# Optimization experiments

Hardware: AMD Instinct MI355X
Metric: run time of the kernel (lower is better)

## Reference

```python
import jax, jax.numpy as jnp
import numpy as np

N, DIM = 8192, 128

def setup_inputs() -> dict:
    key = jax.random.key(0)
    ks = jax.random.split(key, 9)
    s = 1.0 / np.sqrt(DIM)
    return {
        "x": jax.random.normal(ks[0], (N, DIM), dtype=jnp.float32),
        "Wq": jax.random.uniform(ks[1], (DIM, DIM), jnp.float32, -s, s),
        "bq": jax.random.uniform(ks[2], (DIM,), jnp.float32, -s, s),
        "Wk": jax.random.uniform(ks[3], (DIM, DIM), jnp.float32, -s, s),
        "bk": jax.random.uniform(ks[4], (DIM,), jnp.float32, -s, s),
        "Wv": jax.random.uniform(ks[5], (DIM, DIM), jnp.float32, -s, s),
        "bv": jax.random.uniform(ks[6], (DIM,), jnp.float32, -s, s),
        "Wo": jax.random.uniform(ks[7], (DIM, DIM), jnp.float32, -s, s),
        "bo": jax.random.uniform(ks[8], (DIM,), jnp.float32, -s, s),
    }

def reference(x, Wq, bq, Wk, bk, Wv, bv, Wo, bo):
    # nn.Linear: y = x @ W.T + b
    Q = x @ Wq.T + bq                      # [N, d]
    K = x @ Wk.T + bk                      # [N, d]
    V = x @ Wv.T + bv                      # [N, d]
    scale = 1.0 / jnp.sqrt(jnp.asarray(x.shape[-1], x.dtype))
    scores = (Q @ K.T) * scale             # [N, N] — matches original O(n^2) math
    attn = jax.nn.softmax(scores, axis=-1)
    out = attn @ V                         # [N, d]
    return out @ Wo.T + bo
```

## Files before the change

### kernel.cpp

```cpp
#include <hip/hip_runtime.h>
#include <math.h>


typedef __bf16 bf16x8 __attribute__((ext_vector_type(8)));
typedef float f32x4 __attribute__((ext_vector_type(4)));
typedef float f32x16 __attribute__((ext_vector_type(16)));
typedef unsigned int u32x4 __attribute__((ext_vector_type(4)));
typedef unsigned int u32x2 __attribute__((ext_vector_type(2)));
typedef unsigned short us16;

#define NTOK 8192
#define CHUNKS 8

static constexpr float SCALE_L2E = 0.08838834764831845f * 1.4426950408889634f;

__device__ __forceinline__ unsigned f2bf_u(float x) {
    unsigned u = __builtin_bit_cast(unsigned, x);
    return (u + 0x7FFFu + ((u >> 16) & 1u)) >> 16;
}

__device__ __forceinline__ unsigned pk_bf16(float x, float y) {
    unsigned a = __builtin_bit_cast(unsigned, x) + 0x8000u;
    unsigned b = __builtin_bit_cast(unsigned, y) + 0x8000u;
#if __has_builtin(__builtin_amdgcn_perm)
    return __builtin_amdgcn_perm(b, a, 0x07060302u);
#else
    return (a >> 16) | (b & 0xFFFF0000u);
#endif
}

__device__ __forceinline__ unsigned cvtpk_bf16(float x, float y) {
    unsigned r;
    asm("v_cvt_pk_bf16_f32 %0, %1, %2" : "=v"(r) : "v"(x), "v"(y));
    return r;
}

__device__ __forceinline__ void plswap(unsigned& a, unsigned& b) {
    asm("v_permlane32_swap_b32 %0, %1" : "+v"(a), "+v"(b));
}

__device__ __forceinline__ void pl16swap(unsigned& a, unsigned& b) {
    asm("v_permlane16_swap_b32 %0, %1" : "+v"(a), "+v"(b));
}

__device__ __forceinline__ float fexp2(float x) {
#if __has_builtin(__builtin_amdgcn_exp2f)
    return __builtin_amdgcn_exp2f(x);
#else
    return exp2f(x);
#endif
}

__device__ __forceinline__ bf16x8 ld_frag(const us16* p) {
    u32x4 u = *reinterpret_cast<const u32x4*>(p);
    return __builtin_bit_cast(bf16x8, u);
}

__device__ __forceinline__ bf16x8 cvt_frag(const float* p) {
    f32x4 a = *reinterpret_cast<const f32x4*>(p);
    f32x4 b = *reinterpret_cast<const f32x4*>(p + 4);
    u32x4 o;
    o[0] = f2bf_u(a[0]) | (f2bf_u(a[1]) << 16);
    o[1] = f2bf_u(a[2]) | (f2bf_u(a[3]) << 16);
    o[2] = f2bf_u(b[0]) | (f2bf_u(b[1]) << 16);
    o[3] = f2bf_u(b[2]) | (f2bf_u(b[3]) << 16);
    return __builtin_bit_cast(bf16x8, o);
}

__global__ __launch_bounds__(256) void proj_qkv(
    const float* __restrict__ x,
    const float* __restrict__ wq, const float* __restrict__ bq,
    const float* __restrict__ wk, const float* __restrict__ bk,
    const float* __restrict__ wv, const float* __restrict__ bv,
    us16* __restrict__ Qb, us16* __restrict__ Kb, us16* __restrict__ Vt)
{
    __shared__ us16 ldsT[4][16 * 136];

    int z = blockIdx.x >> 7;
    int tile = blockIdx.x & 127;
    const float* W = z == 0 ? wq : z == 1 ? wk : wv;
    const float* bias = z == 0 ? bq : z == 1 ? bk : bv;
    float osc = z == 0 ? SCALE_L2E : 1.0f;

    int w = threadIdx.x >> 6, lane = threadIdx.x & 63;
    int quad = lane >> 4, l15 = lane & 15;
    int rbase = tile * 64 + w * 16;

    bf16x8 af[4];
#pragma unroll
    for (int ks = 0; ks < 4; ++ks)
        af[ks] = cvt_frag(x + (rbase + l15) * 128 + ks * 32 + quad * 8);

    f32x4 acc[8];
#pragma unroll
    for (int nt = 0; nt < 8; ++nt) acc[nt] = f32x4{0.f, 0.f, 0.f, 0.f};

#pragma unroll
    for (int nt = 0; nt < 8; ++nt) {
#pragma unroll
        for (int ks = 0; ks < 4; ++ks) {
            bf16x8 bf = cvt_frag(W + (nt * 16 + l15) * 128 + ks * 32 + quad * 8);
            acc[nt] = __builtin_amdgcn_mfma_f32_16x16x32_bf16(af[ks], bf, acc[nt], 0, 0, 0);
        }
    }

    if (z < 2) {
        us16* T = &ldsT[w][0];
        us16* Out = z == 0 ? Qb : Kb;
#pragma unroll
        for (int nt = 0; nt < 8; ++nt) {
            float bb = bias[nt * 16 + l15];
#pragma unroll
            for (int r = 0; r < 4; ++r)
                T[(quad * 4 + r) * 136 + nt * 16 + l15] =
                    (us16)f2bf_u((acc[nt][r] + bb) * osc);
        }
        asm volatile("s_waitcnt lgkmcnt(0)" ::: "memory");
        __builtin_amdgcn_sched_barrier(0);
        int row = lane >> 2, seg = lane & 3;
        const us16* src = T + row * 136 + seg * 32;
        us16* dst = Out + (rbase + row) * 128 + seg * 32;
#pragma unroll
        for (int c = 0; c < 4; ++c)
            *reinterpret_cast<u32x4*>(dst + c * 8) =
                *reinterpret_cast<const u32x4*>(src + c * 8);
    } else {
#pragma unroll
        for (int nt = 0; nt < 8; ++nt) {
            float bb = bias[nt * 16 + l15];
            int d = nt * 16 + l15, r0 = rbase + quad * 4;
            u32x2 pk;
            pk[0] = f2bf_u(acc[nt][0] + bb) | (f2bf_u(acc[nt][1] + bb) << 16);
            pk[1] = f2bf_u(acc[nt][2] + bb) | (f2bf_u(acc[nt][3] + bb) << 16);
            *reinterpret_cast<u32x2*>(Vt + d * NTOK + r0) = pk;
        }
    }
}

__global__ __launch_bounds__(512, 2) void attn(
    const us16* __restrict__ Qb, const us16* __restrict__ Kb,
    const us16* __restrict__ Vt,
    float* __restrict__ Opart, float* __restrict__ Lpart)
{
    __shared__ us16 ldsK[2][64 * 136];
    __shared__ us16 ldsV[2][128 * 72];

    int qtile = blockIdx.x >> 3, chunk = blockIdx.x & 7;
    int tid = threadIdx.x, w = tid >> 6, lane = tid & 63;
    int quad = lane >> 4, l15 = lane & 15;
    int qb0 = qtile * 256 + w * 32;
    int k0 = chunk * 1024;

    bf16x8 qf[2][4];
#pragma unroll
    for (int mt = 0; mt < 2; ++mt)
#pragma unroll
        for (int ks = 0; ks < 4; ++ks)
            qf[mt][ks] = ld_frag(Qb + (qb0 + mt * 16 + l15) * 128 + ks * 32 + quad * 8);

    f32x4 o[2][8];
#pragma unroll
    for (int mt = 0; mt < 2; ++mt)
#pragma unroll
        for (int dt = 0; dt < 8; ++dt) o[mt][dt] = f32x4{0.f, 0.f, 0.f, 0.f};

    f32x4 lacc[2];
    lacc[0] = f32x4{0.f, 0.f, 0.f, 0.f};
    lacc[1] = f32x4{0.f, 0.f, 0.f, 0.f};

    u32x4 onesu;
    onesu[0] = onesu[1] = onesu[2] = onesu[3] = 0x3F803F80u;
    bf16x8 ones = __builtin_bit_cast(bf16x8, onesu);

#pragma unroll
    for (int c = 0; c < 2; ++c) {
        int idx = tid + c * 512, r = idx >> 4, cc = idx & 15;
        *reinterpret_cast<u32x4*>(&ldsK[0][0] + r * 136 + cc * 8) =
            *reinterpret_cast<const u32x4*>(Kb + (k0 + r) * 128 + cc * 8);
    }
#pragma unroll
    for (int c = 0; c < 2; ++c) {
        int idx = tid + c * 512, r = idx >> 3, cc = idx & 7;
        *reinterpret_cast<u32x4*>(&ldsV[0][0] + r * 72 + cc * 8) =
            *reinterpret_cast<const u32x4*>(Vt + (size_t)r * NTOK + k0 + cc * 8);
    }
    __syncthreads();

    for (int it = 0; it < 16; ++it) {
        int cur = it & 1;
        const us16* K_ = &ldsK[cur][0];
        const us16* V_ = &ldsV[cur][0];

        u32x4 kreg[2], vreg[2];
        if (it < 15) {
            int kk = k0 + (it + 1) * 64;
#pragma unroll
            for (int c = 0; c < 2; ++c) {
                int idx = tid + c * 512, r = idx >> 4, cc = idx & 15;
                kreg[c] = *reinterpret_cast<const u32x4*>(Kb + (kk + r) * 128 + cc * 8);
            }
#pragma unroll
            for (int c = 0; c < 2; ++c) {
                int idx = tid + c * 512, r = idx >> 3, cc = idx & 7;
                vreg[c] = *reinterpret_cast<const u32x4*>(Vt + (size_t)r * NTOK + kk + cc * 8);
            }
            __builtin_amdgcn_sched_barrier(0);
        }

        f32x4 s[2][4];
#pragma unroll
        for (int mt = 0; mt < 2; ++mt)
#pragma unroll
            for (int nt = 0; nt < 4; ++nt) s[mt][nt] = f32x4{0.f, 0.f, 0.f, 0.f};

        __builtin_amdgcn_s_setprio(1);
#pragma unroll
        for (int nt = 0; nt < 4; ++nt) {
#pragma unroll
            for (int ks = 0; ks < 4; ++ks) {
                bf16x8 kf = ld_frag(K_ + (nt * 16 + l15) * 136 + ks * 32 + quad * 8);
                s[0][nt] = __builtin_amdgcn_mfma_f32_16x16x32_bf16(kf, qf[0][ks], s[0][nt], 0, 0, 0);
                s[1][nt] = __builtin_amdgcn_mfma_f32_16x16x32_bf16(kf, qf[1][ks], s[1][nt], 0, 0, 0);
            }
        }
        __builtin_amdgcn_s_setprio(0);

        bf16x8 afP[2][2];
#pragma unroll
        for (int mt = 0; mt < 2; ++mt) {
            unsigned W[4][2];
#pragma unroll
            for (int nt = 0; nt < 4; ++nt) {
                float p0 = fexp2(s[mt][nt][0]);
                float p1 = fexp2(s[mt][nt][1]);
                float p2 = fexp2(s[mt][nt][2]);
                float p3 = fexp2(s[mt][nt][3]);
                W[nt][0] = cvtpk_bf16(p0, p1);
                W[nt][1] = cvtpk_bf16(p2, p3);
            }
#pragma unroll
            for (int k2 = 0; k2 < 2; ++k2) {
                u32x4 f;
                {
                    unsigned X = W[2 * k2][0], Y = W[2 * k2 + 1][0];
                    plswap(X, Y); pl16swap(X, Y);
                    f[0] = X; f[2] = Y;
                }
                {
                    unsigned X = W[2 * k2][1], Y = W[2 * k2 + 1][1];
                    plswap(X, Y); pl16swap(X, Y);
                    f[1] = X; f[3] = Y;
                }
                afP[mt][k2] = __builtin_bit_cast(bf16x8, f);
            }
        }

        lacc[0] = __builtin_amdgcn_mfma_f32_16x16x32_bf16(afP[0][0], ones, lacc[0], 0, 0, 0);
        lacc[0] = __builtin_amdgcn_mfma_f32_16x16x32_bf16(afP[0][1], ones, lacc[0], 0, 0, 0);
        lacc[1] = __builtin_amdgcn_mfma_f32_16x16x32_bf16(afP[1][0], ones, lacc[1], 0, 0, 0);
        lacc[1] = __builtin_amdgcn_mfma_f32_16x16x32_bf16(afP[1][1], ones, lacc[1], 0, 0, 0);

        __builtin_amdgcn_s_setprio(1);
#pragma unroll
        for (int dt = 0; dt < 8; ++dt) {
#pragma unroll
            for (int k2 = 0; k2 < 2; ++k2) {
                bf16x8 bv = ld_frag(V_ + (dt * 16 + l15) * 72 + k2 * 32 + quad * 8);
                o[0][dt] = __builtin_amdgcn_mfma_f32_16x16x32_bf16(afP[0][k2], bv, o[0][dt], 0, 0, 0);
                o[1][dt] = __builtin_amdgcn_mfma_f32_16x16x32_bf16(afP[1][k2], bv, o[1][dt], 0, 0, 0);
            }
        }
        __builtin_amdgcn_s_setprio(0);

        if (it < 15) {
            __builtin_amdgcn_sched_barrier(0);
#pragma unroll
            for (int c = 0; c < 2; ++c) {
                int idx = tid + c * 512, r = idx >> 4, cc = idx & 15;
                *reinterpret_cast<u32x4*>(&ldsK[cur ^ 1][0] + r * 136 + cc * 8) = kreg[c];
            }
#pragma unroll
            for (int c = 0; c < 2; ++c) {
                int idx = tid + c * 512, r = idx >> 3, cc = idx & 7;
                *reinterpret_cast<u32x4*>(&ldsV[cur ^ 1][0] + r * 72 + cc * 8) = vreg[c];
            }
        }
        __syncthreads();
    }

#pragma unroll
    for (int mt = 0; mt < 2; ++mt)
#pragma unroll
        for (int dt = 0; dt < 8; ++dt)
#pragma unroll
            for (int r = 0; r < 4; ++r) {
                int row = qb0 + mt * 16 + quad * 4 + r;
                Opart[(size_t)(chunk * NTOK + row) * 128 + dt * 16 + l15] = o[mt][dt][r];
            }
    if (l15 == 0) {
#pragma unroll
        for (int mt = 0; mt < 2; ++mt)
#pragma unroll
            for (int r = 0; r < 4; ++r) {
                int row = qb0 + mt * 16 + quad * 4 + r;
                Lpart[chunk * NTOK + row] = lacc[mt][r];
            }
    }
}

__global__ __launch_bounds__(256) void combine_proj(
    const float* __restrict__ Opart, const float* __restrict__ Lpart,
    const float* __restrict__ Wo, const float* __restrict__ bo,
    float* __restrict__ out)
{
    __shared__ us16 ldsO[32 * 136];
    __shared__ float ldsL[32];

    int tile = blockIdx.x, t = threadIdx.x;
    int r0 = tile * 32;

    if (t < 32) {
        float L = 0.f;
#pragma unroll
        for (int c = 0; c < CHUNKS; ++c) L += Lpart[c * NTOK + r0 + t];
        ldsL[t] = 1.0f / L;
    }

    f32x4 acc[4];
#pragma unroll
    for (int j = 0; j < 4; ++j) acc[j] = f32x4{0.f, 0.f, 0.f, 0.f};

#pragma unroll
    for (int c = 0; c < CHUNKS; ++c) {
        const float* src = Opart + (size_t)(c * NTOK + r0) * 128;
#pragma unroll
        for (int j = 0; j < 4; ++j) {
            f32x4 v = *reinterpret_cast<const f32x4*>(src + j * 1024 + t * 4);
            acc[j] += v;
        }
    }
    __syncthreads();

#pragma unroll
    for (int j = 0; j < 4; ++j) {
        int flat = j * 1024 + t * 4;
        int row = flat >> 7, col = flat & 127;
        float sc = ldsL[row];
        u32x2 wv;
        wv[0] = pk_bf16(acc[j][0] * sc, acc[j][1] * sc);
        wv[1] = pk_bf16(acc[j][2] * sc, acc[j][3] * sc);
        *reinterpret_cast<u32x2*>(ldsO + row * 136 + col) = wv;
    }
    __syncthreads();

    int w = t >> 6, lane = t & 63;
    int l31 = lane & 31, hi = lane >> 5;

    bf16x8 af[8];
#pragma unroll
    for (int ks = 0; ks < 8; ++ks)
        af[ks] = ld_frag(ldsO + l31 * 136 + ks * 16 + hi * 8);

    f32x16 acc2;
#pragma unroll
    for (int r = 0; r < 16; ++r) acc2[r] = 0.f;

#pragma unroll
    for (int ks = 0; ks < 8; ++ks) {
        bf16x8 bfw = cvt_frag(Wo + (w * 32 + l31) * 128 + ks * 16 + hi * 8);
        acc2 = __builtin_amdgcn_mfma_f32_32x32x16_bf16(af[ks], bfw, acc2, 0, 0, 0);
    }

    float bb = bo[w * 32 + l31];
#pragma unroll
    for (int r = 0; r < 16; ++r) {
        int m = (r & 3) + 8 * (r >> 2) + 4 * hi;
        out[(size_t)(r0 + m) * 128 + w * 32 + l31] = acc2[r] + bb;
    }
}

extern "C" void kernel_launch(void* const* d_in, const int* in_sizes, int n_in,
                              void* d_out, int out_size, void* d_ws, size_t ws_size,
                              hipStream_t stream)
{
    const float* x  = (const float*)d_in[0];
    const float* Wq = (const float*)d_in[1];
    const float* bq = (const float*)d_in[2];
    const float* Wk = (const float*)d_in[3];
    const float* bk = (const float*)d_in[4];
    const float* Wv = (const float*)d_in[5];
    const float* bv = (const float*)d_in[6];
    const float* Wo = (const float*)d_in[7];
    const float* bo = (const float*)d_in[8];

    char* ws = (char*)d_ws;
    const size_t MB = 1024 * 1024;
    us16* Qb  = (us16*)(ws + 0 * MB);
    us16* Kb  = (us16*)(ws + 2 * MB);
    us16* Vt  = (us16*)(ws + 4 * MB);
    float* Lp = (float*)(ws + 6 * MB);
    float* Op = (float*)(ws + 7 * MB);

    proj_qkv<<<384, 256, 0, stream>>>(x, Wq, bq, Wk, bk, Wv, bv, Qb, Kb, Vt);
    attn<<<256, 512, 0, stream>>>(Qb, Kb, Vt, Op, Lp);
    combine_proj<<<256, 256, 0, stream>>>(Op, Lp, Wo, bo, (float*)d_out);
}
```

Before: 138.1 us.

## Fuse QKV projection, attention, and output projection into one cooperative kernel

Replaces three kernel launches with a single cooperative kernel of 256 blocks of 512 threads. Grid-wide syncs separate the projection phase (192 blocks, each doing 128 rows), the attention phase and the combine/output-projection phase, and LDS is shared across phases. The aim is to remove launch gaps and inter-kernel tails. In exchange, the projection and combine phases run at lower parallelism (some blocks idle, half the waves idle in the output GEMM), and each grid barrier costs time.

```diff
diff --git a/kernel.cpp b/kernel.cpp
--- a/kernel.cpp
+++ b/kernel.cpp
@@ -1,5 +1,8 @@
 #include <hip/hip_runtime.h>
+#include <hip/hip_cooperative_groups.h>
 #include <math.h>
+
+namespace cg = cooperative_groups;
 
 
 typedef __bf16 bf16x8 __attribute__((ext_vector_type(8)));
@@ -11,6 +14,8 @@
 
 #define NTOK 8192
 #define CHUNKS 8
+#define KTILE (64 * 136)
+#define VTILE (128 * 72)
 
 static constexpr float SCALE_L2E = 0.08838834764831845f * 1.4426950408889634f;
 
@@ -67,315 +72,321 @@
     return __builtin_bit_cast(bf16x8, o);
 }
 
-__global__ __launch_bounds__(256) void proj_qkv(
+__global__ __launch_bounds__(512, 2) void fused(
     const float* __restrict__ x,
     const float* __restrict__ wq, const float* __restrict__ bq,
     const float* __restrict__ wk, const float* __restrict__ bk,
     const float* __restrict__ wv, const float* __restrict__ bv,
-    us16* __restrict__ Qb, us16* __restrict__ Kb, us16* __restrict__ Vt)
+    const float* __restrict__ Wo, const float* __restrict__ bo,
+    us16* __restrict__ Qb, us16* __restrict__ Kb, us16* __restrict__ Vt,
+    float* __restrict__ Opart, float* __restrict__ Lpart,
+    float* __restrict__ out)
 {
-    __shared__ us16 ldsT[4][16 * 136];
-
-    int z = blockIdx.x >> 7;
-    int tile = blockIdx.x & 127;
-    const float* W = z == 0 ? wq : z == 1 ? wk : wv;
-    const float* bias = z == 0 ? bq : z == 1 ? bk : bv;
-    float osc = z == 0 ? SCALE_L2E : 1.0f;
-
-    int w = threadIdx.x >> 6, lane = threadIdx.x & 63;
-    int quad = lane >> 4, l15 = lane & 15;
-    int rbase = tile * 64 + w * 16;
-
-    bf16x8 af[4];
-#pragma unroll
-    for (int ks = 0; ks < 4; ++ks)
-        af[ks] = cvt_frag(x + (rbase + l15) * 128 + ks * 32 + quad * 8);
-
-    f32x4 acc[8];
-#pragma unroll
-    for (int nt = 0; nt < 8; ++nt) acc[nt] = f32x4{0.f, 0.f, 0.f, 0.f};
-
-#pragma unroll
-    for (int nt = 0; nt < 8; ++nt) {
-#pragma unroll
-        for (int ks = 0; ks < 4; ++ks) {
-            bf16x8 bf = cvt_frag(W + (nt * 16 + l15) * 128 + ks * 32 + quad * 8);
-            acc[nt] = __builtin_amdgcn_mfma_f32_16x16x32_bf16(af[ks], bf, acc[nt], 0, 0, 0);
-        }
-    }
-
-    if (z < 2) {
-        us16* T = &ldsT[w][0];
-        us16* Out = z == 0 ? Qb : Kb;
-#pragma unroll
-        for (int nt = 0; nt < 8; ++nt) {
-            float bb = bias[nt * 16 + l15];
-#pragma unroll
-            for (int r = 0; r < 4; ++r)
-                T[(quad * 4 + r) * 136 + nt * 16 + l15] =
-                    (us16)f2bf_u((acc[nt][r] + bb) * osc);
-        }
-        asm volatile("s_waitcnt lgkmcnt(0)" ::: "memory");
-        __builtin_amdgcn_sched_barrier(0);
-        int row = lane >> 2, seg = lane & 3;
-        const us16* src = T + row * 136 + seg * 32;
-        us16* dst = Out + (rbase + row) * 128 + seg * 32;
-#pragma unroll
-        for (int c = 0; c < 4; ++c)
-            *reinterpret_cast<u32x4*>(dst + c * 8) =
-                *reinterpret_cast<const u32x4*>(src + c * 8);
-    } else {
-#pragma unroll
-        for (int nt = 0; nt < 8; ++nt) {
-            float bb = bias[nt * 16 + l15];
-            int d = nt * 16 + l15, r0 = rbase + quad * 4;
-            u32x2 pk;
-            pk[0] = f2bf_u(acc[nt][0] + bb) | (f2bf_u(acc[nt][1] + bb) << 16);
-            pk[1] = f2bf_u(acc[nt][2] + bb) | (f2bf_u(acc[nt][3] + bb) << 16);
-            *reinterpret_cast<u32x2*>(Vt + d * NTOK + r0) = pk;
-        }
-    }
-}
-
-__global__ __launch_bounds__(512, 2) void attn(
-    const us16* __restrict__ Qb, const us16* __restrict__ Kb,
-    const us16* __restrict__ Vt,
-    float* __restrict__ Opart, float* __restrict__ Lpart)
-{
-    __shared__ us16 ldsK[2][64 * 136];
-    __shared__ us16 ldsV[2][128 * 72];
-
-    int qtile = blockIdx.x >> 3, chunk = blockIdx.x & 7;
+    __shared__ us16 smem[2 * KTILE + 2 * VTILE];
+    __shared__ float ldsL[32];
+
+    cg::grid_group grid = cg::this_grid();
+
+    int bid = blockIdx.x;
     int tid = threadIdx.x, w = tid >> 6, lane = tid & 63;
     int quad = lane >> 4, l15 = lane & 15;
-    int qb0 = qtile * 256 + w * 32;
-    int k0 = chunk * 1024;
-
-    bf16x8 qf[2][4];
-#pragma unroll
-    for (int mt = 0; mt < 2; ++mt)
+
+    if (bid < 192) {
+        int z = bid >> 6;
+        int tile = bid & 63;
+        const float* W = z == 0 ? wq : z == 1 ? wk : wv;
+        const float* bias = z == 0 ? bq : z == 1 ? bk : bv;
+        float osc = z == 0 ? SCALE_L2E : 1.0f;
+        int rbase = tile * 128 + w * 16;
+
+        bf16x8 af[4];
 #pragma unroll
         for (int ks = 0; ks < 4; ++ks)
-            qf[mt][ks] = ld_frag(Qb + (qb0 + mt * 16 + l15) * 128 + ks * 32 + quad * 8);
-
-    f32x4 o[2][8];
-#pragma unroll
-    for (int mt = 0; mt < 2; ++mt)
-#pragma unroll
-        for (int dt = 0; dt < 8; ++dt) o[mt][dt] = f32x4{0.f, 0.f, 0.f, 0.f};
-
-    f32x4 lacc[2];
-    lacc[0] = f32x4{0.f, 0.f, 0.f, 0.f};
-    lacc[1] = f32x4{0.f, 0.f, 0.f, 0.f};
-
-    u32x4 onesu;
-    onesu[0] = onesu[1] = onesu[2] = onesu[3] = 0x3F803F80u;
-    bf16x8 ones = __builtin_bit_cast(bf16x8, onesu);
-
-#pragma unroll
-    for (int c = 0; c < 2; ++c) {
-        int idx = tid + c * 512, r = idx >> 4, cc = idx & 15;
-        *reinterpret_cast<u32x4*>(&ldsK[0][0] + r * 136 + cc * 8) =
-            *reinterpret_cast<const u32x4*>(Kb + (k0 + r) * 128 + cc * 8);
+            af[ks] = cvt_frag(x + (rbase + l15) * 128 + ks * 32 + quad * 8);
+
+        f32x4 acc[8];
+#pragma unroll
+        for (int nt = 0; nt < 8; ++nt) acc[nt] = f32x4{0.f, 0.f, 0.f, 0.f};
+
+#pragma unroll
+        for (int nt = 0; nt < 8; ++nt) {
+#pragma unroll
+            for (int ks = 0; ks < 4; ++ks) {
+                bf16x8 bf = cvt_frag(W + (nt * 16 + l15) * 128 + ks * 32 + quad * 8);
+                acc[nt] = __builtin_amdgcn_mfma_f32_16x16x32_bf16(af[ks], bf, acc[nt], 0, 0, 0);
+            }
+        }
+
+        if (z < 2) {
+            us16* T = smem + w * (16 * 136);
+            us16* Out = z == 0 ? Qb : Kb;
+#pragma unroll
+            for (int nt = 0; nt < 8; ++nt) {
+                float bb = bias[nt * 16 + l15];
+#pragma unroll
+                for (int r = 0; r < 4; ++r)
+                    T[(quad * 4 + r) * 136 + nt * 16 + l15] =
+                        (us16)f2bf_u((acc[nt][r] + bb) * osc);
+            }
+            asm volatile("s_waitcnt lgkmcnt(0)" ::: "memory");
+            __builtin_amdgcn_sched_barrier(0);
+            int row = lane >> 2, seg = lane & 3;
+            const us16* src = T + row * 136 + seg * 32;
+            us16* dst = Out + (rbase + row) * 128 + seg * 32;
+#pragma unroll
+            for (int c = 0; c < 4; ++c)
+                *reinterpret_cast<u32x4*>(dst + c * 8) =
+                    *reinterpret_cast<const u32x4*>(src + c * 8);
+        } else {
+#pragma unroll
+            for (int nt = 0; nt < 8; ++nt) {
+                float bb = bias[nt * 16 + l15];
+                int d = nt * 16 + l15, r0 = rbase + quad * 4;
+                u32x2 pk;
+                pk[0] = f2bf_u(acc[nt][0] + bb) | (f2bf_u(acc[nt][1] + bb) << 16);
+                pk[1] = f2bf_u(acc[nt][2] + bb) | (f2bf_u(acc[nt][3] + bb) << 16);
+                *reinterpret_cast<u32x2*>(Vt + d * NTOK + r0) = pk;
+            }
+        }
     }
-#pragma unroll
-    for (int c = 0; c < 2; ++c) {
-        int idx = tid + c * 512, r = idx >> 3, cc = idx & 7;
-        *reinterpret_cast<u32x4*>(&ldsV[0][0] + r * 72 + cc * 8) =
-            *reinterpret_cast<const u32x4*>(Vt + (size_t)r * NTOK + k0 + cc * 8);
+
+    __threadfence();
+    grid.sync();
+
+    {
+        us16* ldsK0 = smem;
+        us16* ldsV0 = smem + 2 * KTILE;
+
+        int qtile = bid >> 3, chunk = bid & 7;
+        int qb0 = qtile * 256 + w * 32;
+        int k0 = chunk * 1024;
+
+        bf16x8 qf[2][4];
+#pragma unroll
+        for (int mt = 0; mt < 2; ++mt)
+#pragma unroll
+            for (int ks = 0; ks < 4; ++ks)
+                qf[mt][ks] = ld_frag(Qb + (qb0 + mt * 16 + l15) * 128 + ks * 32 + quad * 8);
+
+        f32x4 o[2][8];
+#pragma unroll
+        for (int mt = 0; mt < 2; ++mt)
+#pragma unroll
+            for (int dt = 0; dt < 8; ++dt) o[mt][dt] = f32x4{0.f, 0.f, 0.f, 0.f};
+
+        f32x4 lacc[2];
+        lacc[0] = f32x4{0.f, 0.f, 0.f, 0.f};
+        lacc[1] = f32x4{0.f, 0.f, 0.f, 0.f};
+
+        u32x4 onesu;
+        onesu[0] = onesu[1] = onesu[2] = onesu[3] = 0x3F803F80u;
+        bf16x8 ones = __builtin_bit_cast(bf16x8, onesu);
+
+#pragma unroll
+        for (int c = 0; c < 2; ++c) {
+            int idx = tid + c * 512, r = idx >> 4, cc = idx & 15;
+            *reinterpret_cast<u32x4*>(ldsK0 + r * 136 + cc * 8) =
+                *reinterpret_cast<const u32x4*>(Kb + (k0 + r) * 128 + cc * 8);
+        }
+#pragma unroll
+        for (int c = 0; c < 2; ++c) {
+            int idx = tid + c * 512, r = idx >> 3, cc = idx & 7;
+            *reinterpret_cast<u32x4*>(ldsV0 + r * 72 + cc * 8) =
+                *reinterpret_cast<const u32x4*>(Vt + (size_t)r * NTOK + k0 + cc * 8);
+        }
+        __syncthreads();
+
+        for (int it = 0; it < 16; ++it) {
+            int cur = it & 1;
+            const us16* K_ = ldsK0 + cur * KTILE;
+            const us16* V_ = ldsV0 + cur * VTILE;
+
+            u32x4 kreg[2], vreg[2];
+            if (it < 15) {
+                int kk = k0 + (it + 1) * 64;
+#pragma unroll
+                for (int c = 0; c < 2; ++c) {
+                    int idx = tid + c * 512, r = idx >> 4, cc = idx & 15;
+                    kreg[c] = *reinterpret_cast<const u32x4*>(Kb + (kk + r) * 128 + cc * 8);
+                }
+#pragma unroll
+                for (int c = 0; c < 2; ++c) {
+                    int idx = tid + c * 512, r = idx >> 3, cc = idx & 7;
+                    vreg[c] = *reinterpret_cast<const u32x4*>(Vt + (size_t)r * NTOK + kk + cc * 8);
+                }
+                __builtin_amdgcn_sched_barrier(0);
+            }
+
+            f32x4 s[2][4];
+#pragma unroll
+            for (int mt = 0; mt < 2; ++mt)
+#pragma unroll
+                for (int nt = 0; nt < 4; ++nt) s[mt][nt] = f32x4{0.f, 0.f, 0.f, 0.f};
+
+            __builtin_amdgcn_s_setprio(1);
+#pragma unroll
+            for (int nt = 0; nt < 4; ++nt) {
+#pragma unroll
+                for (int ks = 0; ks < 4; ++ks) {
+                    bf16x8 kf = ld_frag(K_ + (nt * 16 + l15) * 136 + ks * 32 + quad * 8);
+                    s[0][nt] = __builtin_amdgcn_mfma_f32_16x16x32_bf16(kf, qf[0][ks], s[0][nt], 0, 0, 0);
+                    s[1][nt] = __builtin_amdgcn_mfma_f32_16x16x32_bf16(kf, qf[1][ks], s[1][nt], 0, 0, 0);
+                }
+            }
+            __builtin_amdgcn_s_setprio(0);
+
+            bf16x8 afP[2][2];
+#pragma unroll
+            for (int mt = 0; mt < 2; ++mt) {
+                unsigned W[4][2];
+#pragma unroll
+                for (int nt = 0; nt < 4; ++nt) {
+                    float p0 = fexp2(s[mt][nt][0]);
+                    float p1 = fexp2(s[mt][nt][1]);
+                    float p2 = fexp2(s[mt][nt][2]);
+                    float p3 = fexp2(s[mt][nt][3]);
+                    W[nt][0] = cvtpk_bf16(p0, p1);
+                    W[nt][1] = cvtpk_bf16(p2, p3);
+                }
+#pragma unroll
+                for (int k2 = 0; k2 < 2; ++k2) {
+                    u32x4 f;
+                    {
+                        unsigned X = W[2 * k2][0], Y = W[2 * k2 + 1][0];
+                        plswap(X, Y); pl16swap(X, Y);
+                        f[0] = X; f[2] = Y;
+                    }
+                    {
+                        unsigned X = W[2 * k2][1], Y = W[2 * k2 + 1][1];
+                        plswap(X, Y); pl16swap(X, Y);
+                        f[1] = X; f[3] = Y;
+                    }
+                    afP[mt][k2] = __builtin_bit_cast(bf16x8, f);
+                }
+            }
+
+            lacc[0] = __builtin_amdgcn_mfma_f32_16x16x32_bf16(afP[0][0], ones, lacc[0], 0, 0, 0);
+            lacc[0] = __builtin_amdgcn_mfma_f32_16x16x32_bf16(afP[0][1], ones, lacc[0], 0, 0, 0);
+            lacc[1] = __builtin_amdgcn_mfma_f32_16x16x32_bf16(afP[1][0], ones, lacc[1], 0, 0, 0);
+            lacc[1] = __builtin_amdgcn_mfma_f32_16x16x32_bf16(afP[1][1], ones, lacc[1], 0, 0, 0);
+
+            __builtin_amdgcn_s_setprio(1);
+#pragma unroll
+            for (int dt = 0; dt < 8; ++dt) {
+#pragma unroll
+                for (int k2 = 0; k2 < 2; ++k2) {
+                    bf16x8 bv = ld_frag(V_ + (dt * 16 + l15) * 72 + k2 * 32 + quad * 8);
+                    o[0][dt] = __builtin_amdgcn_mfma_f32_16x16x32_bf16(afP[0][k2], bv, o[0][dt], 0, 0, 0);
+                    o[1][dt] = __builtin_amdgcn_mfma_f32_16x16x32_bf16(afP[1][k2], bv, o[1][dt], 0, 0, 0);
+                }
+            }
+            __builtin_amdgcn_s_setprio(0);
+
+            if (it < 15) {
+                __builtin_amdgcn_sched_barrier(0);
+                us16* Kn = ldsK0 + (cur ^ 1) * KTILE;
+                us16* Vn = ldsV0 + (cur ^ 1) * VTILE;
+#pragma unroll
+                for (int c = 0; c < 2; ++c) {
+                    int idx = tid + c * 512, r = idx >> 4, cc = idx & 15;
+                    *reinterpret_cast<u32x4*>(Kn + r * 136 + cc * 8) = kreg[c];
+                }
+#pragma unroll
+                for (int c = 0; c < 2; ++c) {
+                    int idx = tid + c * 512, r = idx >> 3, cc = idx & 7;
+                    *reinterpret_cast<u32x4*>(Vn + r * 72 + cc * 8) = vreg[c];
+                }
+            }
+            __syncthreads();
+        }
+
+#pragma unroll
+        for (int mt = 0; mt < 2; ++mt)
+#pragma unroll
+            for (int dt = 0; dt < 8; ++dt)
+#pragma unroll
+                for (int r = 0; r < 4; ++r) {
+                    int row = qb0 + mt * 16 + quad * 4 + r;
+                    Opart[(size_t)(chunk * NTOK + row) * 128 + dt * 16 + l15] = o[mt][dt][r];
+                }
+        if (l15 == 0) {
+#pragma unroll
+            for (int mt = 0; mt < 2; ++mt)
+#pragma unroll
+                for (int r = 0; r < 4; ++r) {
+                    int row = qb0 + mt * 16 + quad * 4 + r;
+                    Lpart[chunk * NTOK + row] = lacc[mt][r];
+                }
+        }
     }
-    __syncthreads();
-
-    for (int it = 0; it < 16; ++it) {
-        int cur = it & 1;
-        const us16* K_ = &ldsK[cur][0];
-        const us16* V_ = &ldsV[cur][0];
-
-        u32x4 kreg[2], vreg[2];
-        if (it < 15) {
-            int kk = k0 + (it + 1) * 64;
-#pragma unroll
-            for (int c = 0; c < 2; ++c) {
-                int idx = tid + c * 512, r = idx >> 4, cc = idx & 15;
-                kreg[c] = *reinterpret_cast<const u32x4*>(Kb + (kk + r) * 128 + cc * 8);
-            }
-#pragma unroll
-            for (int c = 0; c < 2; ++c) {
-                int idx = tid + c * 512, r = idx >> 3, cc = idx & 7;
-                vreg[c] = *reinterpret_cast<const u32x4*>(Vt + (size_t)r * NTOK + kk + cc * 8);
-            }
-            __builtin_amdgcn_sched_barrier(0);
-        }
-
-        f32x4 s[2][4];
-#pragma unroll
-        for (int mt = 0; mt < 2; ++mt)
-#pragma unroll
-            for (int nt = 0; nt < 4; ++nt) s[mt][nt] = f32x4{0.f, 0.f, 0.f, 0.f};
-
-        __builtin_amdgcn_s_setprio(1);
-#pragma unroll
-        for (int nt = 0; nt < 4; ++nt) {
-#pragma unroll
-            for (int ks = 0; ks < 4; ++ks) {
-                bf16x8 kf = ld_frag(K_ + (nt * 16 + l15) * 136 + ks * 32 + quad * 8);
-                s[0][nt] = __builtin_amdgcn_mfma_f32_16x16x32_bf16(kf, qf[0][ks], s[0][nt], 0, 0, 0);
-                s[1][nt] = __builtin_amdgcn_mfma_f32_16x16x32_bf16(kf, qf[1][ks], s[1][nt], 0, 0, 0);
-            }
-        }
-        __builtin_amdgcn_s_setprio(0);
-
-        bf16x8 afP[2][2];
-#pragma unroll
-        for (int mt = 0; mt < 2; ++mt) {
-            unsigned W[4][2];
-#pragma unroll
-            for (int nt = 0; nt < 4; ++nt) {
-                float p0 = fexp2(s[mt][nt][0]);
-                float p1 = fexp2(s[mt][nt][1]);
-                float p2 = fexp2(s[mt][nt][2]);
-                float p3 = fexp2(s[mt][nt][3]);
-                W[nt][0] = cvtpk_bf16(p0, p1);
-                W[nt][1] = cvtpk_bf16(p2, p3);
-            }
-#pragma unroll
-            for (int k2 = 0; k2 < 2; ++k2) {
-                u32x4 f;
-                {
-                    unsigned X = W[2 * k2][0], Y = W[2 * k2 + 1][0];
-                    plswap(X, Y); pl16swap(X, Y);
-                    f[0] = X; f[2] = Y;
-                }
-                {
-                    unsigned X = W[2 * k2][1], Y = W[2 * k2 + 1][1];
-                    plswap(X, Y); pl16swap(X, Y);
-                    f[1] = X; f[3] = Y;
-                }
-                afP[mt][k2] = __builtin_bit_cast(bf16x8, f);
-            }
-        }
-
-        lacc[0] = __builtin_amdgcn_mfma_f32_16x16x32_bf16(afP[0][0], ones, lacc[0], 0, 0, 0);
-        lacc[0] = __builtin_amdgcn_mfma_f32_16x16x32_bf16(afP[0][1], ones, lacc[0], 0, 0, 0);
-        lacc[1] = __builtin_amdgcn_mfma_f32_16x16x32_bf16(afP[1][0], ones, lacc[1], 0, 0, 0);
-        lacc[1] = __builtin_amdgcn_mfma_f32_16x16x32_bf16(afP[1][1], ones, lacc[1], 0, 0, 0);
-
-        __builtin_amdgcn_s_setprio(1);
-#pragma unroll
-        for (int dt = 0; dt < 8; ++dt) {
-#pragma unroll
-            for (int k2 = 0; k2 < 2; ++k2) {
-                bf16x8 bv = ld_frag(V_ + (dt * 16 + l15) * 72 + k2 * 32 + quad * 8);
-                o[0][dt] = __builtin_amdgcn_mfma_f32_16x16x32_bf16(afP[0][k2], bv, o[0][dt], 0, 0, 0);
-                o[1][dt] = __builtin_amdgcn_mfma_f32_16x16x32_bf16(afP[1][k2], bv, o[1][dt], 0, 0, 0);
-            }
-        }
-        __builtin_amdgcn_s_setprio(0);
-
-        if (it < 15) {
-            __builtin_amdgcn_sched_barrier(0);
-#pragma unroll
-            for (int c = 0; c < 2; ++c) {
-                int idx = tid + c * 512, r = idx >> 4, cc = idx & 15;
-                *reinterpret_cast<u32x4*>(&ldsK[cur ^ 1][0] + r * 136 + cc * 8) = kreg[c];
-            }
-#pragma unroll
-            for (int c = 0; c < 2; ++c) {
-                int idx = tid + c * 512, r = idx >> 3, cc = idx & 7;
-                *reinterpret_cast<u32x4*>(&ldsV[cur ^ 1][0] + r * 72 + cc * 8) = vreg[c];
+
+    __threadfence();
+    grid.sync();
+
+    {
+        us16* ldsO = smem;
+        int r0 = bid * 32;
+        int t = tid;
+
+        if (t < 32) {
+            float L = 0.f;
+#pragma unroll
+            for (int c = 0; c < CHUNKS; ++c) L += Lpart[c * NTOK + r0 + t];
+            ldsL[t] = 1.0f / L;
+        }
+
+        f32x4 acc[2];
+        acc[0] = f32x4{0.f, 0.f, 0.f, 0.f};
+        acc[1] = f32x4{0.f, 0.f, 0.f, 0.f};
+
+#pragma unroll
+        for (int c = 0; c < CHUNKS; ++c) {
+            const float* src = Opart + (size_t)(c * NTOK + r0) * 128;
+#pragma unroll
+            for (int j = 0; j < 2; ++j) {
+                f32x4 v = *reinterpret_cast<const f32x4*>(src + j * 2048 + t * 4);
+                acc[j] += v;
             }
         }
         __syncthreads();
-    }
-
-#pragma unroll
-    for (int mt = 0; mt < 2; ++mt)
-#pragma unroll
-        for (int dt = 0; dt < 8; ++dt)
-#pragma unroll
-            for (int r = 0; r < 4; ++r) {
-                int row = qb0 + mt * 16 + quad * 4 + r;
-                Opart[(size_t)(chunk * NTOK + row) * 128 + dt * 16 + l15] = o[mt][dt][r];
-            }
-    if (l15 == 0) {
-#pragma unroll
-        for (int mt = 0; mt < 2; ++mt)
-#pragma unroll
-            for (int r = 0; r < 4; ++r) {
-                int row = qb0 + mt * 16 + quad * 4 + r;
-                Lpart[chunk * NTOK + row] = lacc[mt][r];
-            }
-    }
-}
-
-__global__ __launch_bounds__(256) void combine_proj(
-    const float* __restrict__ Opart, const float* __restrict__ Lpart,
-    const float* __restrict__ Wo, const float* __restrict__ bo,
-    float* __restrict__ out)
-{
-    __shared__ us16 ldsO[32 * 136];
-    __shared__ float ldsL[32];
-
-    int tile = blockIdx.x, t = threadIdx.x;
-    int r0 = tile * 32;
-
-    if (t < 32) {
-        float L = 0.f;
-#pragma unroll
-        for (int c = 0; c < CHUNKS; ++c) L += Lpart[c * NTOK + r0 + t];
-        ldsL[t] = 1.0f / L;
-    }
-
-    f32x4 acc[4];
-#pragma unroll
-    for (int j = 0; j < 4; ++j) acc[j] = f32x4{0.f, 0.f, 0.f, 0.f};
-
-#pragma unroll
-    for (int c = 0; c < CHUNKS; ++c) {
-        const float* src = Opart + (size_t)(c * NTOK + r0) * 128;
-#pragma unroll
-        for (int j = 0; j < 4; ++j) {
-            f32x4 v = *reinterpret_cast<const f32x4*>(src + j * 1024 + t * 4);
-            acc[j] += v;
-        }
-    }
-    __syncthreads();
-
-#pragma unroll
-    for (int j = 0; j < 4; ++j) {
-        int flat = j * 1024 + t * 4;
-        int row = flat >> 7, col = flat & 127;
-        float sc = ldsL[row];
-        u32x2 wv;
-        wv[0] = pk_bf16(acc[j][0] * sc, acc[j][1] * sc);
-        wv[1] = pk_bf16(acc[j][2] * sc, acc[j][3] * sc);
-        *reinterpret_cast<u32x2*>(ldsO + row * 136 + col) = wv;
-    }
-    __syncthreads();
-
-    int w = t >> 6, lane = t & 63;
-    int l31 = lane & 31, hi = lane >> 5;
-
-    bf16x8 af[8];
-#pragma unroll
-    for (int ks = 0; ks < 8; ++ks)
-        af[ks] = ld_frag(ldsO + l31 * 136 + ks * 16 + hi * 8);
-
-    f32x16 acc2;
-#pragma unroll
-    for (int r = 0; r < 16; ++r) acc2[r] = 0.f;
-
-#pragma unroll
-    for (int ks = 0; ks < 8; ++ks) {
-        bf16x8 bfw = cvt_frag(Wo + (w * 32 + l31) * 128 + ks * 16 + hi * 8);
-        acc2 = __builtin_amdgcn_mfma_f32_32x32x16_bf16(af[ks], bfw, acc2, 0, 0, 0);
-    }
-
-    float bb = bo[w * 32 + l31];
-#pragma unroll
-    for (int r = 0; r < 16; ++r) {
-        int m = (r & 3) + 8 * (r >> 2) + 4 * hi;
-        out[(size_t)(r0 + m) * 128 + w * 32 + l31] = acc2[r] + bb;
+
+#pragma unroll
+        for (int j = 0; j < 2; ++j) {
+            int flat = j * 2048 + t * 4;
+            int row = flat >> 7, col = flat & 127;
+            float sc = ldsL[row];
+            u32x2 wv;
+            wv[0] = pk_bf16(acc[j][0] * sc, acc[j][1] * sc);
+            wv[1] = pk_bf16(acc[j][2] * sc, acc[j][3] * sc);
+            *reinterpret_cast<u32x2*>(ldsO + row * 136 + col) = wv;
+        }
+        __syncthreads();
+
+        if (w < 4) {
+            int l31 = lane & 31, hi = lane >> 5;
+
+            bf16x8 af[8];
+#pragma unroll
+            for (int ks = 0; ks < 8; ++ks)
+                af[ks] = ld_frag(ldsO + l31 * 136 + ks * 16 + hi * 8);
+
+            f32x16 acc2;
+#pragma unroll
+            for (int r = 0; r < 16; ++r) acc2[r] = 0.f;
+
+#pragma unroll
+            for (int ks = 0; ks < 8; ++ks) {
+                bf16x8 bfw = cvt_frag(Wo + (w * 32 + l31) * 128 + ks * 16 + hi * 8);
+                acc2 = __builtin_amdgcn_mfma_f32_32x32x16_bf16(af[ks], bfw, acc2, 0, 0, 0);
+            }
+
+            float bb = bo[w * 32 + l31];
+#pragma unroll
+            for (int r = 0; r < 16; ++r) {
+                int m = (r & 3) + 8 * (r >> 2) + 4 * hi;
+                out[(size_t)(r0 + m) * 128 + w * 32 + l31] = acc2[r] + bb;
+            }
+        }
     }
 }
 
@@ -400,8 +411,10 @@
     us16* Vt  = (us16*)(ws + 4 * MB);
     float* Lp = (float*)(ws + 6 * MB);
     float* Op = (float*)(ws + 7 * MB);
-
-    proj_qkv<<<384, 256, 0, stream>>>(x, Wq, bq, Wk, bk, Wv, bv, Qb, Kb, Vt);
-    attn<<<256, 512, 0, stream>>>(Qb, Kb, Vt, Op, Lp);
-    combine_proj<<<256, 256, 0, stream>>>(Op, Lp, Wo, bo, (float*)d_out);
-}
+    float* outp = (float*)d_out;
+
+    void* args[] = { &x, &Wq, &bq, &Wk, &bk, &Wv, &bv, &Wo, &bo,
+                     &Qb, &Kb, &Vt, &Op, &Lp, &outp };
+    (void)hipLaunchCooperativeKernel((void*)fused, dim3(256), dim3(512),
+                                     args, 0, stream);
+}
```

Measured after the change: 345.8 us. +150.4%, slower.
